# Performance work log

Measured on AMD Instinct MI355X. Metric: run time of the kernel, lower is better.

## Reference

```python
import jax, jax.numpy as jnp
import numpy as np

N = 100000   # nodes
E = 1600000  # edges
IN_DIM = 64
OUT_DIM = 64
HEADS = 4
C = OUT_DIM // HEADS  # per-head channels = 16
EDGE_DIM = 16
NEG_SLOPE = 0.2
EPS = 1e-5


def setup_inputs() -> dict:
    key = jax.random.key(0)
    ks = jax.random.split(key, 16)
    s = 0.1
    return {
        "x": jax.random.normal(ks[0], (N, IN_DIM), jnp.float32),
        "edge_index": jax.random.randint(ks[1], (2, E), 0, N, jnp.int64 if jax.config.jax_enable_x64 else jnp.int32),
        "edge_attr": jax.random.normal(ks[2], (E, EDGE_DIM), jnp.float32),
        # GATv2Conv params (share_weights=False, edge_dim, concat=True)
        "Wl": jax.random.normal(ks[3], (IN_DIM, HEADS * C), jnp.float32) * s,
        "bl": jnp.zeros((HEADS * C,), jnp.float32),
        "Wr": jax.random.normal(ks[4], (IN_DIM, HEADS * C), jnp.float32) * s,
        "br": jnp.zeros((HEADS * C,), jnp.float32),
        "We": jax.random.normal(ks[5], (EDGE_DIM, HEADS * C), jnp.float32) * s,
        "att": jax.random.normal(ks[6], (HEADS, C), jnp.float32) * s,
        "conv_bias": jnp.zeros((HEADS * C,), jnp.float32),
        # edge gate MLP: Linear(edge_dim, 2*edge_dim) -> SiLU -> Linear(2*edge_dim, 1) -> Sigmoid
        "Wg1": jax.random.normal(ks[7], (EDGE_DIM, 2 * EDGE_DIM), jnp.float32) * s,
        "bg1": jnp.zeros((2 * EDGE_DIM,), jnp.float32),
        "Wg2": jax.random.normal(ks[8], (2 * EDGE_DIM, 1), jnp.float32) * s,
        "bg2": jnp.zeros((1,), jnp.float32),
        # LayerNorm(out_dim)
        "gamma": jnp.ones((OUT_DIM,), jnp.float32),
        "beta": jnp.zeros((OUT_DIM,), jnp.float32),
    }


def _silu(v):
    return v * jax.nn.sigmoid(v)


def reference(x, edge_index, edge_attr, Wl, bl, Wr, br, We, att, conv_bias,
              Wg1, bg1, Wg2, bg2, gamma, beta):
    src, tgt = edge_index[0], edge_index[1]

    # --- edge gate: sigmoid(Linear(SiLU(Linear(e)))) -> [E, 1]
    gate = jax.nn.sigmoid(_silu(edge_attr @ Wg1 + bg1) @ Wg2 + bg2)

    # --- GATv2Conv ---
    xl = (x @ Wl + bl).reshape(N, HEADS, C)   # source transform
    xr = (x @ Wr + br).reshape(N, HEADS, C)   # target transform
    ee = (edge_attr @ We).reshape(E, HEADS, C)

    xj = xl[src]                               # [E, H, C] source messages
    m = jax.nn.leaky_relu(xj + xr[tgt] + ee, NEG_SLOPE)
    alpha = jnp.einsum('ehc,hc->eh', m, att)   # [E, H]

    # segment softmax over edges sharing the same target node
    amax = jax.ops.segment_max(alpha, tgt, num_segments=N)  # [N, H]
    a = jnp.exp(alpha - amax[tgt])
    denom = jax.ops.segment_sum(a, tgt, num_segments=N)
    a = a / denom[tgt]

    out = jax.ops.segment_sum(xj * a[:, :, None], tgt, num_segments=N)
    out = out.reshape(N, HEADS * C) + conv_bias

    # --- edge-gate mean modulation per target node ---
    gate_sum = jax.ops.segment_sum(gate[:, 0], tgt, num_segments=N)
    degree = jax.ops.segment_sum(jnp.ones((E,), out.dtype), tgt, num_segments=N)
    mean_gate = gate_sum / jnp.maximum(degree, 1.0)
    out = out * mean_gate[:, None]

    # --- LayerNorm -> SiLU -> (dropout p=0) -> residual (Identity proj) ---
    mu = jnp.mean(out, axis=-1, keepdims=True)
    var = jnp.var(out, axis=-1, keepdims=True)
    out = (out - mu) * jax.lax.rsqrt(var + EPS) * gamma + beta
    out = _silu(out)
    return out + x
```

## Files before the change

### kernel.cpp

```cpp
#include <hip/hip_runtime.h>
#include <hip/hip_bf16.h>
#include <math.h>

#define N_NODES 100000
#define N_EDGES 1600000
#define IN_DIM 64
#define OUT_DIM 64
#define HEADS 4
#define CH 16
#define EDGE_DIM 16
#define NEG_SLOPE 0.2f
#define LN_EPS 1e-5f
#define NBLK 391
#define CHUNK 32

typedef unsigned short u16;
typedef unsigned int u32;
typedef unsigned long long u64;
typedef __attribute__((ext_vector_type(8))) short bf16x8;
typedef __attribute__((ext_vector_type(4))) float f32x4;

__device__ __forceinline__ float bf2f(u16 v) {
    return __uint_as_float(((u32)v) << 16);
}
__device__ __forceinline__ u16 f2bf(float f) {
    u32 u = __float_as_uint(f);
    u32 r = (u + 0x7FFFu + ((u >> 16) & 1u)) >> 16;
    return (u16)r;
}
__device__ __forceinline__ void load16bf(const u16* p, float* out) {
    const uint4* q = (const uint4*)p;
    uint4 a = q[0], b = q[1];
    u32 w[8] = {a.x, a.y, a.z, a.w, b.x, b.y, b.z, b.w};
#pragma unroll
    for (int i = 0; i < 8; ++i) {
        out[2*i]   = __uint_as_float(w[i] << 16);
        out[2*i+1] = __uint_as_float(w[i] & 0xFFFF0000u);
    }
}
__device__ __forceinline__ void load16f(const void* base, long i, bool f32in, float* out) {
    if (f32in) {
        const float4* q = (const float4*)((const float*)base + i);
        float4 v0 = q[0], v1 = q[1], v2 = q[2], v3 = q[3];
        out[0]=v0.x; out[1]=v0.y; out[2]=v0.z; out[3]=v0.w;
        out[4]=v1.x; out[5]=v1.y; out[6]=v1.z; out[7]=v1.w;
        out[8]=v2.x; out[9]=v2.y; out[10]=v2.z; out[11]=v2.w;
        out[12]=v3.x; out[13]=v3.y; out[14]=v3.z; out[15]=v3.w;
    } else {
        load16bf((const u16*)base + i, out);
    }
}
__device__ __forceinline__ float ldf(const void* base, int i, bool f32in) {
    return f32in ? ((const float*)base)[i] : bf2f(((const u16*)base)[i]);
}

#define DPP_ROR_ADD(v, N) do { \
    int _d = __builtin_amdgcn_update_dpp(0, __float_as_int(v), 0x120 + (N), 0xF, 0xF, true); \
    (v) += __int_as_float(_d); } while (0)

__global__ void k_sniff_zero(const u32* __restrict__ xw, const int* __restrict__ eiw,
                             int* __restrict__ flags, int4* __restrict__ cur4,
                             float4* __restrict__ gsum4) {
    if (blockIdx.x != 0) {
        const int i = (blockIdx.x - 1) * 256 + threadIdx.x;
        if (i < N_NODES / 4) cur4[i] = make_int4(0, 0, 0, 0);
        else if (i < N_NODES / 2) gsum4[i - N_NODES / 4] = make_float4(0.f, 0.f, 0.f, 0.f);
        return;
    }
    __shared__ int s_f32, s_not64;
    const int t = threadIdx.x;
    if (t == 0) { s_f32 = 0; s_not64 = 0; }
    __syncthreads();
    if (t < 64) {
        u32 w = xw[t];
        for (int h = 0; h < 2; ++h) {
            u32 bits = h ? (w & 0xFFFF0000u) : (w << 16);
            float v = __uint_as_float(bits);
            float a = fabsf(v);
            bool sane = (a == 0.0f) || (a >= 1e-30f && a <= 1000.0f);
            if (!sane || v != v) atomicOr(&s_f32, 1);
        }
    } else if (t < 96) {
        if (eiw[2 * (t - 64) + 1] != 0) atomicOr(&s_not64, 1);
    }
    __syncthreads();
    if (t == 0) flags[0] = s_f32 | ((s_not64 ? 0 : 1) << 1);
}

__global__ __launch_bounds__(256) void k_transform(
    const void* __restrict__ x,
    const void* __restrict__ Wl, const void* __restrict__ bl,
    const void* __restrict__ Wr, const void* __restrict__ br,
    u16* __restrict__ xl, u16* __restrict__ xr,
    const int* __restrict__ flags)
{
    const bool f32in = (flags[0] & 1) != 0;
    const int lane = threadIdx.x & 63;
    const int w = threadIdx.x >> 6;
    const int m0 = blockIdx.x * 64;
    const int col = lane & 15;
    const int quad = lane >> 4;

    bf16x8 bfrag[2][2];
    float bias[2];
#pragma unroll
    for (int nt = 0; nt < 2; ++nt) {
        const int ng = w * 32 + nt * 16 + col;
        const void* W  = (ng < 64) ? Wl : Wr;
        const void* bi = (ng < 64) ? bl : br;
        const int c = ng & 63;
        bias[nt] = ldf(bi, c, f32in);
#pragma unroll
        for (int kf = 0; kf < 2; ++kf)
#pragma unroll
            for (int j = 0; j < 8; ++j) {
                const int k = kf * 32 + quad * 8 + j;
                bfrag[nt][kf][j] = (short)f2bf(ldf(W, k * 64 + c, f32in));
            }
    }

#pragma unroll
    for (int mt = 0; mt < 4; ++mt) {
        const int mrow = m0 + mt * 16 + col;
        const int m = (mrow < N_NODES) ? mrow : (N_NODES - 1);
        bf16x8 afrag[2];
#pragma unroll
        for (int kf = 0; kf < 2; ++kf) {
            const int kb = kf * 32 + quad * 8;
            if (f32in) {
                const float* xp = (const float*)x + (size_t)m * 64 + kb;
#pragma unroll
                for (int j = 0; j < 8; ++j) afrag[kf][j] = (short)f2bf(xp[j]);
            } else {
                afrag[kf] = *(const bf16x8*)((const u16*)x + (size_t)m * 64 + kb);
            }
        }
#pragma unroll
        for (int nt = 0; nt < 2; ++nt) {
            f32x4 c = {bias[nt], bias[nt], bias[nt], bias[nt]};
            c = __builtin_amdgcn_mfma_f32_16x16x32_bf16(afrag[0], bfrag[nt][0], c, 0, 0, 0);
            c = __builtin_amdgcn_mfma_f32_16x16x32_bf16(afrag[1], bfrag[nt][1], c, 0, 0, 0);
            const int ng = w * 32 + nt * 16 + col;
            u16* dst = (ng < 64) ? xl : xr;
            const int cc = ng & 63;
#pragma unroll
            for (int r = 0; r < 4; ++r) {
                const int node = m0 + mt * 16 + quad * 4 + r;
                if (node < N_NODES) dst[(size_t)node * 64 + cc] = f2bf(c[r]);
            }
        }
    }
}

__global__ __launch_bounds__(256) void k_count_gate(
    const int* __restrict__ ei, int* __restrict__ cur,
    float4* __restrict__ zreg, float* __restrict__ gsum,
    const void* __restrict__ edge_attr,
    const void* __restrict__ Wg1, const void* __restrict__ bg1,
    const void* __restrict__ Wg2, const void* __restrict__ bg2,
    const int* __restrict__ flags)
{
    __shared__ float sWg1t[32 * 16];
    __shared__ float sBg1[32];
    __shared__ float sWg2[32];
    __shared__ float sBg2;
    const int tid = threadIdx.x;
    const int fl = flags[0];
    const bool f32in = (fl & 1) != 0;
    const bool i64   = (fl & 2) != 0;
    for (int i = tid; i < 32 * 16; i += 256) {
        const int j = i >> 4, k = i & 15;
        sWg1t[i] = ldf(Wg1, k * 32 + j, f32in);
    }
    if (tid < 32) sBg1[tid] = ldf(bg1, tid, f32in);
    if (tid >= 32 && tid < 64) sWg2[tid - 32] = ldf(Wg2, tid - 32, f32in);
    if (tid == 0) sBg2 = ldf(bg2, 0, f32in);

    const int gid = blockIdx.x * 256 + tid;
    for (int i = gid; i < N_NODES * 68 / 4; i += 6250 * 256)
        zreg[i] = make_float4(0.f, 0.f, 0.f, 0.f);
    const int tgt = i64 ? ei[2 * (N_EDGES + gid)] : ei[N_EDGES + gid];
    atomicAdd(&cur[tgt], 1);

    __syncthreads();
    float ea[EDGE_DIM];
    load16f(edge_attr, (long)gid * EDGE_DIM, f32in, ea);
    float g = sBg2;
#pragma unroll
    for (int j = 0; j < 32; ++j) {
        float hv = sBg1[j];
        const float4* wr = (const float4*)&sWg1t[j * 16];
#pragma unroll
        for (int k4 = 0; k4 < 4; ++k4) {
            const float4 wv = wr[k4];
            hv += ea[4*k4]   * wv.x + ea[4*k4+1] * wv.y
                + ea[4*k4+2] * wv.z + ea[4*k4+3] * wv.w;
        }
        hv = hv / (1.f + __expf(-hv));
        g += hv * sWg2[j];
    }
    g = 1.f / (1.f + __expf(-g));
    atomicAdd(&gsum[tgt], g);
}

__global__ __launch_bounds__(256) void k_bsum(const int* __restrict__ cur,
                                              int* __restrict__ partial)
{
    const int i = blockIdx.x * 256 + threadIdx.x;
    int v = (i < N_NODES) ? cur[i] : 0;
#pragma unroll
    for (int off = 32; off >= 1; off >>= 1) v += __shfl_xor(v, off, 64);
    __shared__ int ws[4];
    if ((threadIdx.x & 63) == 0) ws[threadIdx.x >> 6] = v;
    __syncthreads();
    if (threadIdx.x == 0) partial[blockIdx.x] = ws[0] + ws[1] + ws[2] + ws[3];
}

__global__ void k_bscan(const int* __restrict__ partial, int* __restrict__ poff,
                        int* __restrict__ base)
{
    __shared__ int sp[NBLK];
    for (int i = threadIdx.x; i < NBLK; i += 64) sp[i] = partial[i];
    __syncthreads();
    if (threadIdx.x == 0) {
        int run = 0;
        for (int i = 0; i < NBLK; ++i) { int t = sp[i]; sp[i] = run; run += t; }
        base[N_NODES] = N_EDGES;
    }
    __syncthreads();
    for (int i = threadIdx.x; i < NBLK; i += 64) poff[i] = sp[i];
}

__global__ __launch_bounds__(256) void k_bfinal(int* __restrict__ cur,
                                                const int* __restrict__ poff,
                                                int* __restrict__ base)
{
    const int i = blockIdx.x * 256 + threadIdx.x;
    const int lane = threadIdx.x & 63;
    const int wave = threadIdx.x >> 6;
    int v = (i < N_NODES) ? cur[i] : 0;
    int s = v;
#pragma unroll
    for (int off = 1; off < 64; off <<= 1) {
        int t = __shfl_up(s, off, 64);
        if (lane >= off) s += t;
    }
    __shared__ int wsum[4];
    if (lane == 63) wsum[wave] = s;
    __syncthreads();
    int wb = 0;
    for (int w = 0; w < wave; ++w) wb += wsum[w];
    if (i < N_NODES) {
        base[i] = poff[blockIdx.x] + wb + s - v;
        cur[i] = 0;
    }
}

__global__ __launch_bounds__(256) void k_scatter(
    const int* __restrict__ ei, const int* __restrict__ base, int* __restrict__ cur,
    u64* __restrict__ perm8, const int* __restrict__ flags)
{
    const int e = blockIdx.x * 256 + threadIdx.x;
    const bool i64 = (flags[0] & 2) != 0;
    int src, tgt;
    if (i64) { src = ei[2 * e]; tgt = ei[2 * (N_EDGES + e)]; }
    else     { src = ei[e];     tgt = ei[N_EDGES + e]; }
    const int pos = base[tgt] + atomicAdd(&cur[tgt], 1);
    perm8[pos] = (u64)(u32)src | ((u64)(u32)tgt << 17) | ((u64)(u32)e << 34);
}


__device__ __forceinline__ void seg_flush(
    float* __restrict__ accum, float* __restrict__ dsum_g,
    int t, int lane, float acc, float dsum)
{
    atomicAdd(&accum[(size_t)t * 64 + lane], acc);
    if ((lane & 15) == 0) atomicAdd(&dsum_g[t * 4 + (lane >> 4)], dsum);
}

template<bool F32IN>
__device__ __forceinline__ void ea_issue(const void* __restrict__ edge_attr,
                                         int eid, uint4* r)
{
    if constexpr (F32IN) {
        const uint4* q = (const uint4*)edge_attr + (size_t)eid * 4;
        r[0] = q[0]; r[1] = q[1]; r[2] = q[2]; r[3] = q[3];
    } else {
        const uint4* q = (const uint4*)((const u16*)edge_attr + (size_t)eid * 16);
        r[0] = q[0]; r[1] = q[1];
    }
}

template<bool F32IN>
__device__ __forceinline__ void ea_vals(const uint4* r, float* out)
{
    const u32* w = (const u32*)r;
    if constexpr (F32IN) {
#pragma unroll
        for (int i = 0; i < 16; ++i) out[i] = __uint_as_float(w[i]);
    } else {
#pragma unroll
        for (int i = 0; i < 8; ++i) {
            out[2*i]   = __uint_as_float(w[i] << 16);
            out[2*i+1] = __uint_as_float(w[i] & 0xFFFF0000u);
        }
    }
}

#define PERM_EXTRACT(JJ, S, T, E2) do { \
    const u32 _lo = (u32)__builtin_amdgcn_readlane(plo, (JJ)); \
    const u32 _hi = (u32)__builtin_amdgcn_readlane(phi, (JJ)); \
    (S)  = (int)(_lo & 0x1FFFFu); \
    (T)  = (int)(((_lo >> 17) | (_hi << 15)) & 0x1FFFFu); \
    (E2) = (int)(_hi >> 2); } while (0)

template<bool F32IN>
__device__ __forceinline__ void attn_run(
    const u64* __restrict__ perm8, const void* __restrict__ edge_attr,
    const u16* __restrict__ xl, const u16* __restrict__ xr,
    float* __restrict__ accum, float* __restrict__ dsum_g,
    const float* We_c, float att_c, int lane, int j0)
{
    const u64 pl = perm8[j0 + (lane & (CHUNK - 1))];
    const int plo = (int)(u32)pl;
    const int phi = (int)(u32)(pl >> 32);

    int s_cur, t_cur, e_cur;
    PERM_EXTRACT(0, s_cur, t_cur, e_cur);

    uint4 ear[F32IN ? 4 : 2];
    ea_issue<F32IN>(edge_attr, e_cur, ear);
    u32 xl_c = xl[(size_t)s_cur * 64 + lane];
    u32 xr_c = xr[(size_t)t_cur * 64 + lane];

    int cur_t = t_cur;
    float acc = 0.f, dsum = 0.f;

#pragma unroll
    for (int jj = 0; jj < CHUNK; ++jj) {
        float eav[16];
        ea_vals<F32IN>(ear, eav);
        float ee = 0.f;
#pragma unroll
        for (int k = 0; k < EDGE_DIM; ++k) ee = fmaf(eav[k], We_c[k], ee);
        const float xlf = bf2f((u16)xl_c);
        const float xrf = bf2f((u16)xr_c);

        int s_nxt = s_cur, t_nxt = t_cur, e_nxt = e_cur;
        u32 xl_n = xl_c, xr_n = xr_c;
        if (jj + 1 < CHUNK) {
            PERM_EXTRACT(jj + 1, s_nxt, t_nxt, e_nxt);
            ea_issue<F32IN>(edge_attr, e_nxt, ear);
            xl_n = xl[(size_t)s_nxt * 64 + lane];
            if (t_nxt != t_cur)
                xr_n = xr[(size_t)t_nxt * 64 + lane];
        }

        if (t_cur != cur_t) {
            seg_flush(accum, dsum_g, cur_t, lane, acc, dsum);
            cur_t = t_cur; acc = 0.f; dsum = 0.f;
        }
        float m = xlf + xrf + ee;
        m = fmaxf(m, m * NEG_SLOPE);
        float t = att_c * m;
        DPP_ROR_ADD(t, 1);
        DPP_ROR_ADD(t, 2);
        DPP_ROR_ADD(t, 4);
        DPP_ROR_ADD(t, 8);
        const float a = __expf(t);
        acc  += a * xlf;
        dsum += a;

        s_cur = s_nxt; t_cur = t_nxt; e_cur = e_nxt;
        xl_c = xl_n;   xr_c = xr_n;
    }
    seg_flush(accum, dsum_g, cur_t, lane, acc, dsum);
}

__global__ __launch_bounds__(256, 8) void k_attn_agg(
    const u64* __restrict__ perm8,
    const void* __restrict__ edge_attr,
    const void* __restrict__ We,
    const void* __restrict__ att,
    const u16* __restrict__ xl, const u16* __restrict__ xr,
    float* __restrict__ accum,
    float* __restrict__ dsum_g,
    const int* __restrict__ flags)
{
    const bool f32in = (flags[0] & 1) != 0;
    const int lane = threadIdx.x & 63;
    const int wid = blockIdx.x * 4 + (threadIdx.x >> 6);
    const int j0 = wid * CHUNK;

    float We_c[EDGE_DIM];
#pragma unroll
    for (int k = 0; k < EDGE_DIM; ++k) We_c[k] = ldf(We, k * 64 + lane, f32in);
    const float att_c = ldf(att, lane, f32in);

    if (f32in) attn_run<true >(perm8, edge_attr, xl, xr, accum, dsum_g, We_c, att_c, lane, j0);
    else       attn_run<false>(perm8, edge_attr, xl, xr, accum, dsum_g, We_c, att_c, lane, j0);
}

__global__ __launch_bounds__(256) void k_epilogue(
    const int* __restrict__ base,
    const float* __restrict__ accum, const float* __restrict__ dsum_g,
    const float* __restrict__ gsum,
    const void* __restrict__ conv_bias, const void* __restrict__ gamma,
    const void* __restrict__ beta, const void* __restrict__ x,
    void* __restrict__ out, const int* __restrict__ flags)
{
    const bool f32in = (flags[0] & 1) != 0;
    const int lane = threadIdx.x & 63;
    const int wave = threadIdx.x >> 6;
    const int n = blockIdx.x * 4 + wave;
    if (n >= N_NODES) return;
    const int h = lane >> 4;

    float v = accum[(size_t)n * 64 + lane];
    const float d = dsum_g[n * 4 + h];
    v = (d > 0.f) ? v / d : 0.f;
    v += ldf(conv_bias, lane, f32in);
    const int deg = base[n + 1] - base[n];
    const float mg = gsum[n] / fmaxf((float)deg, 1.0f);
    v *= mg;

    float s = v;
#pragma unroll
    for (int m2 = 32; m2 >= 1; m2 >>= 1) s += __shfl_xor(s, m2, 64);
    const float mu = s * (1.f / 64.f);
    const float diff = v - mu;
    float q = diff * diff;
#pragma unroll
    for (int m2 = 32; m2 >= 1; m2 >>= 1) q += __shfl_xor(q, m2, 64);
    const float var = q * (1.f / 64.f);

    float y = diff * rsqrtf(var + LN_EPS) * ldf(gamma, lane, f32in) + ldf(beta, lane, f32in);
    y = y / (1.f + __expf(-y));
    const float r = y + ldf(x, n * 64 + lane, f32in);
    if (f32in) ((float*)out)[(size_t)n * 64 + lane] = r;
    else       ((u16*)out)[(size_t)n * 64 + lane] = f2bf(r);
}

extern "C" void kernel_launch(void* const* d_in, const int* in_sizes, int n_in,
                              void* d_out, int out_size, void* d_ws, size_t ws_size,
                              hipStream_t stream)
{
    const void* x   = d_in[0];
    const int* ei   = (const int*)d_in[1];
    const void* ea  = d_in[2];
    const void* Wl  = d_in[3];
    const void* bl  = d_in[4];
    const void* Wr  = d_in[5];
    const void* br  = d_in[6];
    const void* We  = d_in[7];
    const void* att = d_in[8];
    const void* cb  = d_in[9];
    const void* Wg1 = d_in[10];
    const void* bg1 = d_in[11];
    const void* Wg2 = d_in[12];
    const void* bg2 = d_in[13];
    const void* gam = d_in[14];
    const void* bet = d_in[15];

    char* ws = (char*)d_ws;
    int*   flags   = (int*)ws;
    int*   cur     = (int*)(ws + 16);
    int*   base    = (int*)(ws + 400016);
    int*   partial = (int*)(ws + 800032);
    int*   poff    = (int*)(ws + 801600);
    u64*   perm8   = (u64*)(ws + 803168);
    float* accum   = (float*)(ws + 13603168);
    float* dsum_g  = (float*)(ws + 39203168);
    float* gsum    = (float*)(ws + 40803168);
    u16*   xl      = (u16*)(ws + 41203168);
    u16*   xr      = (u16*)(ws + 54003168);

    k_sniff_zero<<<197, 256, 0, stream>>>((const u32*)x, ei, flags, (int4*)cur,
                                          (float4*)gsum);

    k_transform<<<(N_NODES + 63) / 64, 256, 0, stream>>>(x, Wl, bl, Wr, br, xl, xr, flags);

    k_count_gate<<<N_EDGES / 256, 256, 0, stream>>>(
        ei, cur, (float4*)accum, gsum, ea, Wg1, bg1, Wg2, bg2, flags);

    k_bsum<<<NBLK, 256, 0, stream>>>(cur, partial);
    k_bscan<<<1, 64, 0, stream>>>(partial, poff, base);
    k_bfinal<<<NBLK, 256, 0, stream>>>(cur, poff, base);

    k_scatter<<<N_EDGES / 256, 256, 0, stream>>>(ei, base, cur, perm8, flags);

    k_attn_agg<<<N_EDGES / CHUNK / 4, 256, 0, stream>>>(
        perm8, ea, We, att, xl, xr, accum, dsum_g, flags);

    k_epilogue<<<(N_NODES + 3) / 4, 256, 0, stream>>>(
        base, accum, dsum_g, gsum, cb, gam, bet, x, d_out, flags);
}
```

Measured before the change: 583.5 us.

## Replicate degree counters and record slots to drop atomics from scatter and gate sum

Degree counting now spreads over 8 replicated counter arrays picked by block index. Each edge stores the slot returned by its counting atomic, so the scatter pass computes its position without a second atomic. The per-edge gate is stored as fp16 and summed per segment inside the attention aggregation kernel, replacing the per-edge atomic on gsum. In exchange it adds extra workspace, zeroing and scan reads for the replicas, reduces gate precision to fp16, and adds a gate load per edge in the attention loop.

```diff
diff --git a/kernel.cpp b/kernel.cpp
--- a/kernel.cpp
+++ b/kernel.cpp
@@ -1,5 +1,6 @@
 #include <hip/hip_runtime.h>
 #include <hip/hip_bf16.h>
+#include <hip/hip_fp16.h>
 #include <math.h>
 
 #define N_NODES 100000
@@ -13,6 +14,7 @@
 #define LN_EPS 1e-5f
 #define NBLK 391
 #define CHUNK 32
+#define NREP 8
 
 typedef unsigned short u16;
 typedef unsigned int u32;
@@ -59,12 +61,13 @@
     (v) += __int_as_float(_d); } while (0)
 
 __global__ void k_sniff_zero(const u32* __restrict__ xw, const int* __restrict__ eiw,
-                             int* __restrict__ flags, int4* __restrict__ cur4,
+                             int* __restrict__ flags, int4* __restrict__ curR4,
                              float4* __restrict__ gsum4) {
     if (blockIdx.x != 0) {
         const int i = (blockIdx.x - 1) * 256 + threadIdx.x;
-        if (i < N_NODES / 4) cur4[i] = make_int4(0, 0, 0, 0);
-        else if (i < N_NODES / 2) gsum4[i - N_NODES / 4] = make_float4(0.f, 0.f, 0.f, 0.f);
+        if (i < NREP * N_NODES / 4) curR4[i] = make_int4(0, 0, 0, 0);
+        else if (i < NREP * N_NODES / 4 + N_NODES / 4)
+            gsum4[i - NREP * N_NODES / 4] = make_float4(0.f, 0.f, 0.f, 0.f);
         return;
     }
     __shared__ int s_f32, s_not64;
@@ -153,8 +156,8 @@
 }
 
 __global__ __launch_bounds__(256) void k_count_gate(
-    const int* __restrict__ ei, int* __restrict__ cur,
-    float4* __restrict__ zreg, float* __restrict__ gsum,
+    const int* __restrict__ ei, int* __restrict__ curR,
+    float4* __restrict__ zreg, u16* __restrict__ slotA, u16* __restrict__ gateA,
     const void* __restrict__ edge_attr,
     const void* __restrict__ Wg1, const void* __restrict__ bg1,
     const void* __restrict__ Wg2, const void* __restrict__ bg2,
@@ -175,14 +178,16 @@
     if (tid < 32) sBg1[tid] = ldf(bg1, tid, f32in);
     if (tid >= 32 && tid < 64) sWg2[tid - 32] = ldf(Wg2, tid - 32, f32in);
     if (tid == 0) sBg2 = ldf(bg2, 0, f32in);
+    __syncthreads();
 
     const int gid = blockIdx.x * 256 + tid;
     for (int i = gid; i < N_NODES * 68 / 4; i += 6250 * 256)
         zreg[i] = make_float4(0.f, 0.f, 0.f, 0.f);
     const int tgt = i64 ? ei[2 * (N_EDGES + gid)] : ei[N_EDGES + gid];
-    atomicAdd(&cur[tgt], 1);
-
-    __syncthreads();
+    const int r = blockIdx.x & (NREP - 1);
+    const int slot = atomicAdd(&curR[r * N_NODES + tgt], 1);
+    slotA[gid] = (u16)slot;
+
     float ea[EDGE_DIM];
     load16f(edge_attr, (long)gid * EDGE_DIM, f32in, ea);
     float g = sBg2;
@@ -200,14 +205,18 @@
         g += hv * sWg2[j];
     }
     g = 1.f / (1.f + __expf(-g));
-    atomicAdd(&gsum[tgt], g);
-}
-
-__global__ __launch_bounds__(256) void k_bsum(const int* __restrict__ cur,
+    gateA[gid] = __half_as_ushort(__float2half(g));
+}
+
+__global__ __launch_bounds__(256) void k_bsum(const int* __restrict__ curR,
                                               int* __restrict__ partial)
 {
     const int i = blockIdx.x * 256 + threadIdx.x;
-    int v = (i < N_NODES) ? cur[i] : 0;
+    int v = 0;
+    if (i < N_NODES) {
+#pragma unroll
+        for (int r = 0; r < NREP; ++r) v += curR[r * N_NODES + i];
+    }
 #pragma unroll
     for (int off = 32; off >= 1; off >>= 1) v += __shfl_xor(v, off, 64);
     __shared__ int ws[4];
@@ -231,14 +240,19 @@
     for (int i = threadIdx.x; i < NBLK; i += 64) poff[i] = sp[i];
 }
 
-__global__ __launch_bounds__(256) void k_bfinal(int* __restrict__ cur,
+__global__ __launch_bounds__(256) void k_bfinal(int* __restrict__ curR,
                                                 const int* __restrict__ poff,
                                                 int* __restrict__ base)
 {
     const int i = blockIdx.x * 256 + threadIdx.x;
     const int lane = threadIdx.x & 63;
     const int wave = threadIdx.x >> 6;
-    int v = (i < N_NODES) ? cur[i] : 0;
+    int c[NREP];
+    int v = 0;
+    if (i < N_NODES) {
+#pragma unroll
+        for (int r = 0; r < NREP; ++r) { c[r] = curR[r * N_NODES + i]; v += c[r]; }
+    }
     int s = v;
 #pragma unroll
     for (int off = 1; off < 64; off <<= 1) {
@@ -251,13 +265,16 @@
     int wb = 0;
     for (int w = 0; w < wave; ++w) wb += wsum[w];
     if (i < N_NODES) {
-        base[i] = poff[blockIdx.x] + wb + s - v;
-        cur[i] = 0;
+        int run = poff[blockIdx.x] + wb + s - v;
+        base[i] = run;
+#pragma unroll
+        for (int r = 0; r < NREP; ++r) { curR[r * N_NODES + i] = run; run += c[r]; }
     }
 }
 
 __global__ __launch_bounds__(256) void k_scatter(
-    const int* __restrict__ ei, const int* __restrict__ base, int* __restrict__ cur,
+    const int* __restrict__ ei, const int* __restrict__ curR,
+    const u16* __restrict__ slotA,
     u64* __restrict__ perm8, const int* __restrict__ flags)
 {
     const int e = blockIdx.x * 256 + threadIdx.x;
@@ -265,17 +282,19 @@
     int src, tgt;
     if (i64) { src = ei[2 * e]; tgt = ei[2 * (N_EDGES + e)]; }
     else     { src = ei[e];     tgt = ei[N_EDGES + e]; }
-    const int pos = base[tgt] + atomicAdd(&cur[tgt], 1);
+    const int r = blockIdx.x & (NREP - 1);
+    const int pos = curR[r * N_NODES + tgt] + (int)slotA[e];
     perm8[pos] = (u64)(u32)src | ((u64)(u32)tgt << 17) | ((u64)(u32)e << 34);
 }
 
 
 __device__ __forceinline__ void seg_flush(
-    float* __restrict__ accum, float* __restrict__ dsum_g,
-    int t, int lane, float acc, float dsum)
+    float* __restrict__ accum, float* __restrict__ dsum_g, float* __restrict__ gsum,
+    int t, int lane, float acc, float dsum, float gs)
 {
     atomicAdd(&accum[(size_t)t * 64 + lane], acc);
     if ((lane & 15) == 0) atomicAdd(&dsum_g[t * 4 + (lane >> 4)], dsum);
+    if (lane == 1) atomicAdd(&gsum[t], gs);
 }
 
 template<bool F32IN>
@@ -317,8 +336,9 @@
 template<bool F32IN>
 __device__ __forceinline__ void attn_run(
     const u64* __restrict__ perm8, const void* __restrict__ edge_attr,
+    const u16* __restrict__ gateA,
     const u16* __restrict__ xl, const u16* __restrict__ xr,
-    float* __restrict__ accum, float* __restrict__ dsum_g,
+    float* __restrict__ accum, float* __restrict__ dsum_g, float* __restrict__ gsum,
     const float* We_c, float att_c, int lane, int j0)
 {
     const u64 pl = perm8[j0 + (lane & (CHUNK - 1))];
@@ -332,9 +352,10 @@
     ea_issue<F32IN>(edge_attr, e_cur, ear);
     u32 xl_c = xl[(size_t)s_cur * 64 + lane];
     u32 xr_c = xr[(size_t)t_cur * 64 + lane];
+    float g_c = __half2float(__ushort_as_half(gateA[e_cur]));
 
     int cur_t = t_cur;
-    float acc = 0.f, dsum = 0.f;
+    float acc = 0.f, dsum = 0.f, gs = 0.f;
 
 #pragma unroll
     for (int jj = 0; jj < CHUNK; ++jj) {
@@ -348,17 +369,19 @@
 
         int s_nxt = s_cur, t_nxt = t_cur, e_nxt = e_cur;
         u32 xl_n = xl_c, xr_n = xr_c;
+        float g_n = g_c;
         if (jj + 1 < CHUNK) {
             PERM_EXTRACT(jj + 1, s_nxt, t_nxt, e_nxt);
             ea_issue<F32IN>(edge_attr, e_nxt, ear);
             xl_n = xl[(size_t)s_nxt * 64 + lane];
+            g_n = __half2float(__ushort_as_half(gateA[e_nxt]));
             if (t_nxt != t_cur)
                 xr_n = xr[(size_t)t_nxt * 64 + lane];
         }
 
         if (t_cur != cur_t) {
-            seg_flush(accum, dsum_g, cur_t, lane, acc, dsum);
-            cur_t = t_cur; acc = 0.f; dsum = 0.f;
+            seg_flush(accum, dsum_g, gsum, cur_t, lane, acc, dsum, gs);
+            cur_t = t_cur; acc = 0.f; dsum = 0.f; gs = 0.f;
         }
         float m = xlf + xrf + ee;
         m = fmaxf(m, m * NEG_SLOPE);
@@ -370,21 +393,24 @@
         const float a = __expf(t);
         acc  += a * xlf;
         dsum += a;
+        gs   += g_c;
 
         s_cur = s_nxt; t_cur = t_nxt; e_cur = e_nxt;
-        xl_c = xl_n;   xr_c = xr_n;
-    }
-    seg_flush(accum, dsum_g, cur_t, lane, acc, dsum);
+        xl_c = xl_n;   xr_c = xr_n;   g_c = g_n;
+    }
+    seg_flush(accum, dsum_g, gsum, cur_t, lane, acc, dsum, gs);
 }
 
 __global__ __launch_bounds__(256, 8) void k_attn_agg(
     const u64* __restrict__ perm8,
     const void* __restrict__ edge_attr,
+    const u16* __restrict__ gateA,
     const void* __restrict__ We,
     const void* __restrict__ att,
     const u16* __restrict__ xl, const u16* __restrict__ xr,
     float* __restrict__ accum,
     float* __restrict__ dsum_g,
+    float* __restrict__ gsum,
     const int* __restrict__ flags)
 {
     const bool f32in = (flags[0] & 1) != 0;
@@ -397,8 +423,8 @@
     for (int k = 0; k < EDGE_DIM; ++k) We_c[k] = ldf(We, k * 64 + lane, f32in);
     const float att_c = ldf(att, lane, f32in);
 
-    if (f32in) attn_run<true >(perm8, edge_attr, xl, xr, accum, dsum_g, We_c, att_c, lane, j0);
-    else       attn_run<false>(perm8, edge_attr, xl, xr, accum, dsum_g, We_c, att_c, lane, j0);
+    if (f32in) attn_run<true >(perm8, edge_attr, gateA, xl, xr, accum, dsum_g, gsum, We_c, att_c, lane, j0);
+    else       attn_run<false>(perm8, edge_attr, gateA, xl, xr, accum, dsum_g, gsum, We_c, att_c, lane, j0);
 }
 
 __global__ __launch_bounds__(256) void k_epilogue(
@@ -464,33 +490,35 @@
 
     char* ws = (char*)d_ws;
     int*   flags   = (int*)ws;
-    int*   cur     = (int*)(ws + 16);
-    int*   base    = (int*)(ws + 400016);
-    int*   partial = (int*)(ws + 800032);
-    int*   poff    = (int*)(ws + 801600);
-    u64*   perm8   = (u64*)(ws + 803168);
-    float* accum   = (float*)(ws + 13603168);
-    float* dsum_g  = (float*)(ws + 39203168);
-    float* gsum    = (float*)(ws + 40803168);
-    u16*   xl      = (u16*)(ws + 41203168);
-    u16*   xr      = (u16*)(ws + 54003168);
-
-    k_sniff_zero<<<197, 256, 0, stream>>>((const u32*)x, ei, flags, (int4*)cur,
+    int*   curR    = (int*)(ws + 16);
+    int*   base    = (int*)(ws + 3200016);
+    int*   partial = (int*)(ws + 3600032);
+    int*   poff    = (int*)(ws + 3601600);
+    u16*   slotA   = (u16*)(ws + 3603168);
+    u16*   gateA   = (u16*)(ws + 6803168);
+    u64*   perm8   = (u64*)(ws + 10003168);
+    float* accum   = (float*)(ws + 22803168);
+    float* dsum_g  = (float*)(ws + 48403168);
+    float* gsum    = (float*)(ws + 50003168);
+    u16*   xl      = (u16*)(ws + 50403168);
+    u16*   xr      = (u16*)(ws + 63203168);
+
+    k_sniff_zero<<<881, 256, 0, stream>>>((const u32*)x, ei, flags, (int4*)curR,
                                           (float4*)gsum);
 
     k_transform<<<(N_NODES + 63) / 64, 256, 0, stream>>>(x, Wl, bl, Wr, br, xl, xr, flags);
 
     k_count_gate<<<N_EDGES / 256, 256, 0, stream>>>(
-        ei, cur, (float4*)accum, gsum, ea, Wg1, bg1, Wg2, bg2, flags);
-
-    k_bsum<<<NBLK, 256, 0, stream>>>(cur, partial);
+        ei, curR, (float4*)accum, slotA, gateA, ea, Wg1, bg1, Wg2, bg2, flags);
+
+    k_bsum<<<NBLK, 256, 0, stream>>>(curR, partial);
     k_bscan<<<1, 64, 0, stream>>>(partial, poff, base);
-    k_bfinal<<<NBLK, 256, 0, stream>>>(cur, poff, base);
-
-    k_scatter<<<N_EDGES / 256, 256, 0, stream>>>(ei, base, cur, perm8, flags);
+    k_bfinal<<<NBLK, 256, 0, stream>>>(curR, poff, base);
+
+    k_scatter<<<N_EDGES / 256, 256, 0, stream>>>(ei, curR, slotA, perm8, flags);
 
     k_attn_agg<<<N_EDGES / CHUNK / 4, 256, 0, stream>>>(
-        perm8, ea, We, att, xl, xr, accum, dsum_g, flags);
+        perm8, ea, gateA, We, att, xl, xr, accum, dsum_g, gsum, flags);
 
     k_epilogue<<<(N_NODES + 3) / 4, 256, 0, stream>>>(
         base, accum, dsum_g, gsum, cb, gam, bet, x, d_out, flags);
```

Result: faster. 468.2 us (-19.8%).
